# Performance work log

Hardware: AMD Instinct MI355X
Metric: run time of the kernel (lower is better)

## Reference

```python
import jax, jax.numpy as jnp
import numpy as np

B, T, C, H = 4, 2048, 1024, 16
D = C // H  # head_dim = 64

def setup_inputs() -> dict:
    key = jax.random.key(0)
    k1, k2, k3 = jax.random.split(key, 3)
    x = jax.random.normal(k1, (B, T, C), dtype=jnp.float32)
    Wqkv = jax.random.normal(k2, (C, 3 * C), dtype=jnp.float32) * (C ** -0.5)
    Wout = jax.random.normal(k3, (C, C), dtype=jnp.float32) * (C ** -0.5)
    return {"x": x, "Wqkv": Wqkv, "Wout": Wout}

def reference(x, Wqkv, Wout):
    b, t, c = x.shape
    scale = D ** -0.5
    qkv = x @ Wqkv  # [B,T,3C]
    q, k, v = jnp.split(qkv, 3, axis=-1)
    # [B,H,T,D]
    q = q.reshape(b, t, H, D).transpose(0, 2, 1, 3)
    k = k.reshape(b, t, H, D).transpose(0, 2, 1, 3)
    v = v.reshape(b, t, H, D).transpose(0, 2, 1, 3)
    scores = jnp.einsum('bhqd,bhkd->bhqk', q, k) * scale
    causal = jnp.tril(jnp.ones((t, t), dtype=bool))
    scores = jnp.where(causal, scores, -jnp.inf)
    attn = jax.nn.softmax(scores, axis=-1)
    out = jnp.einsum('bhqk,bhkd->bhqd', attn, v)
    out = out.transpose(0, 2, 1, 3).reshape(b, t, c)
    return out @ Wout
```

## Files before the change

kernel.cpp:

```cpp
#include <hip/hip_runtime.h>
#include <hip/hip_bf16.h>

#define DEV __device__ __forceinline__

typedef __attribute__((ext_vector_type(4))) float f32x4;
typedef __attribute__((ext_vector_type(8))) __bf16 bf16x8;
typedef __attribute__((ext_vector_type(8))) unsigned short u16x8;
typedef __attribute__((ext_vector_type(4))) unsigned short u16x4;

DEV unsigned short f2b(float x) {
  unsigned int u = __builtin_bit_cast(unsigned int, x);
  unsigned int r = (u + 0x7fffu + ((u >> 16) & 1u)) >> 16;
  return (unsigned short)r;
}

DEV unsigned int cvtpk(float a, float b) {
  unsigned int r;
  asm("v_cvt_pk_bf16_f32 %0, %1, %2" : "=v"(r) : "v"(a), "v"(b));
  return r;
}

DEV f32x4 mfma16(u16x8 a, u16x8 b, f32x4 c) {
  return __builtin_amdgcn_mfma_f32_16x16x32_bf16(
      __builtin_bit_cast(bf16x8, a), __builtin_bit_cast(bf16x8, b), c, 0, 0, 0);
}

DEV void async16(const unsigned short* g, unsigned short* l) {
  __builtin_amdgcn_global_load_lds(
      (const __attribute__((address_space(1))) void*)g,
      (__attribute__((address_space(3))) void*)l, 16, 0, 0);
}


__global__ void k_convert(const float* __restrict__ in, unsigned short* __restrict__ out, int n8) {
  int i = blockIdx.x * 256 + threadIdx.x;
  if (i >= n8) return;
  const float4* p = (const float4*)in + (size_t)i * 2;
  float4 a = p[0], b = p[1];
  u16x8 v;
  v[0] = f2b(a.x); v[1] = f2b(a.y); v[2] = f2b(a.z); v[3] = f2b(a.w);
  v[4] = f2b(b.x); v[5] = f2b(b.y); v[6] = f2b(b.z); v[7] = f2b(b.w);
  *((u16x8*)out + i) = v;
}

__global__ void k_transpose(const float* __restrict__ in, unsigned short* __restrict__ out,
                            int R, int Cc) {
  __shared__ float tile[32][33];
  int bx = blockIdx.x * 32, by = blockIdx.y * 32;
  int tx = threadIdx.x, ty = threadIdx.y;
#pragma unroll
  for (int i = 0; i < 32; i += 8)
    tile[ty + i][tx] = in[(size_t)(by + ty + i) * Cc + bx + tx];
  __syncthreads();
#pragma unroll
  for (int i = 0; i < 32; i += 8)
    out[(size_t)(bx + ty + i) * R + by + tx] = f2b(tile[tx][ty + i]);
}


template <typename OutT>
__global__ __launch_bounds__(256, 2)
void k_gemm_bt(const unsigned short* __restrict__ A, const unsigned short* __restrict__ Bt,
               OutT* __restrict__ C, int M, int N, int K, int ldc) {
  __shared__ __align__(16) unsigned short As[128 * 32];
  __shared__ __align__(16) unsigned short Bs[128 * 32];
  const int tid = threadIdx.x;
  const int w = tid >> 6, l = tid & 63;
  const int wr = w >> 1, wc = w & 1;
  const int lo = l & 15, hi = l >> 4;
  const int m0 = blockIdx.y * 128, n0 = blockIdx.x * 128;
  const int srow = l >> 2;
  const int scol = (l & 3) * 8;
  const size_t a_base = (size_t)(m0 + 2 * w * 16 + srow) * K + scol;
  const size_t b_base = (size_t)(n0 + 2 * w * 16 + srow) * K + scol;

  f32x4 acc[4][4] = {};

  for (int kt = 0; kt < K; kt += 32) {
    async16(A + a_base + kt, &As[(2 * w) * 512]);
    async16(A + a_base + kt + (size_t)16 * K, &As[(2 * w + 1) * 512]);
    async16(Bt + b_base + kt, &Bs[(2 * w) * 512]);
    async16(Bt + b_base + kt + (size_t)16 * K, &Bs[(2 * w + 1) * 512]);
    __syncthreads();
    u16x8 af[4], bfv[4];
#pragma unroll
    for (int mi = 0; mi < 4; ++mi)
      af[mi] = *(const u16x8*)&As[(wr * 64 + mi * 16 + lo) * 32 + hi * 8];
#pragma unroll
    for (int ni = 0; ni < 4; ++ni)
      bfv[ni] = *(const u16x8*)&Bs[(wc * 64 + ni * 16 + lo) * 32 + hi * 8];
#pragma unroll
    for (int mi = 0; mi < 4; ++mi)
#pragma unroll
      for (int ni = 0; ni < 4; ++ni)
        acc[mi][ni] = mfma16(af[mi], bfv[ni], acc[mi][ni]);
    __syncthreads();
  }
#pragma unroll
  for (int mi = 0; mi < 4; ++mi) {
#pragma unroll
    for (int ni = 0; ni < 4; ++ni) {
      int col = n0 + wc * 64 + ni * 16 + lo;
#pragma unroll
      for (int r = 0; r < 4; ++r) {
        int row = m0 + wr * 64 + mi * 16 + hi * 4 + r;
        float v = acc[mi][ni][r];
        if constexpr (sizeof(OutT) == 4)
          C[(size_t)row * ldc + col] = v;
        else
          C[(size_t)row * ldc + col] = f2b(v);
      }
    }
  }
}


__global__ void k_repack_qk(const unsigned short* __restrict__ qkv,
                            unsigned short* __restrict__ q, unsigned short* __restrict__ k) {
  int idx = blockIdx.x * 256 + threadIdx.x;
  int sel = idx >> 20;
  int rem = idx & ((1 << 20) - 1);
  int m = rem >> 7;
  int ch = rem & 127;
  int h = ch >> 3, d0 = (ch & 7) * 8;
  u16x8 v = *(const u16x8*)&qkv[(size_t)m * 3072 + sel * 1024 + h * 64 + d0];
  int b = m >> 11, t = m & 2047;
  unsigned short* dst = (sel == 0 ? q : k);
  *(u16x8*)&dst[(((size_t)(b * 16 + h)) * 2048 + t) * 64 + d0] = v;
}


__global__ void k_transpose_v(const unsigned short* __restrict__ qkv,
                              unsigned short* __restrict__ vt) {
  __shared__ __align__(16) unsigned short tile[64][68];
  int bh = blockIdx.x >> 5, tt = blockIdx.x & 31;
  int b = bh >> 4, h = bh & 15;
  int t0 = tt * 64;
  int tid = threadIdx.x;
  int rr = tid >> 4, cc = (tid & 15) * 4;
#pragma unroll
  for (int i = 0; i < 4; ++i) {
    int row = rr + i * 16;
    u16x4 v = *(const u16x4*)&qkv[(size_t)(b * 2048 + t0 + row) * 3072 + 2048 + h * 64 + cc];
    *(u16x4*)&tile[row][cc] = v;
  }
  __syncthreads();
  const int c32 = cc & 31;
  const int sbase = (c32 < 16) ? (2 * c32) : (2 * (c32 - 16) + 4);
  const int pos = t0 + (cc >> 5) * 32 + sbase;
#pragma unroll
  for (int i = 0; i < 4; ++i) {
    int d = rr + i * 16;
    u16x4 v;
#pragma unroll
    for (int j = 0; j < 4; ++j) v[j] = tile[cc + j][d];
    *(u16x4*)&vt[((size_t)bh * 64 + d) * 2048 + t0 + pos - t0] = v;
  }
}


DEV void attn_strip(const unsigned short* __restrict__ Q,
                    const unsigned short* __restrict__ Kp,
                    const unsigned short* __restrict__ Vp,
                    unsigned short* __restrict__ AO,
                    int bh, int q0, int lo, int g) {
  const size_t base = (size_t)bh * 2048 * 64;
  const unsigned short* Kb = Kp + base;
  const unsigned short* Vb = Vp + base;

  u16x8 qf[2][2];
#pragma unroll
  for (int qh = 0; qh < 2; ++qh)
#pragma unroll
    for (int dh = 0; dh < 2; ++dh)
      qf[qh][dh] = *(const u16x8*)&Q[base + (size_t)(q0 + qh * 16 + lo) * 64 + dh * 32 + g * 8];

  f32x4 o[2][4] = {};
  float m[2] = {-INFINITY, -INFINITY};
  float lsum[2] = {0.f, 0.f};

  const int nb = q0 / 32 + 1;
  u16x8 kA[2][2], kN[2][2];
#pragma unroll
  for (int kvh = 0; kvh < 2; ++kvh)
#pragma unroll
    for (int dh = 0; dh < 2; ++dh)
      kA[kvh][dh] = *(const u16x8*)&Kb[(size_t)(kvh * 16 + lo) * 64 + dh * 32 + g * 8];

  for (int blk = 0; blk < nb; ++blk) {
    const int kv0 = blk * 32;
    if (blk + 1 < nb) {
      const int kn = kv0 + 32;
#pragma unroll
      for (int kvh = 0; kvh < 2; ++kvh)
#pragma unroll
        for (int dh = 0; dh < 2; ++dh)
          kN[kvh][dh] = *(const u16x8*)&Kb[(size_t)(kn + kvh * 16 + lo) * 64 + dh * 32 + g * 8];
    }
    u16x8 vf[4];
#pragma unroll
    for (int n = 0; n < 4; ++n)
      vf[n] = *(const u16x8*)&Vb[(size_t)(n * 16 + lo) * 2048 + kv0 + g * 8];

    f32x4 sT[2][2];
#pragma unroll
    for (int qh = 0; qh < 2; ++qh)
#pragma unroll
      for (int kvh = 0; kvh < 2; ++kvh) {
        f32x4 z = {};
        z = mfma16(kA[kvh][0], qf[qh][0], z);
        z = mfma16(kA[kvh][1], qf[qh][1], z);
        sT[qh][kvh] = z;
      }

    const bool lastblk = (blk == nb - 1);
#pragma unroll
    for (int qh = 0; qh < 2; ++qh) {
      float s[8];
#pragma unroll
      for (int kvh = 0; kvh < 2; ++kvh)
#pragma unroll
        for (int r = 0; r < 4; ++r)
          s[kvh * 4 + r] = sT[qh][kvh][r] * 0.125f;
      if (lastblk) {
        const int qi = qh * 16 + lo;
#pragma unroll
        for (int kvh = 0; kvh < 2; ++kvh)
#pragma unroll
          for (int r = 0; r < 4; ++r)
            if (kvh * 16 + 4 * g + r > qi) s[kvh * 4 + r] = -INFINITY;
      }
      float mx = fmaxf(fmaxf(fmaxf(s[0], s[1]), fmaxf(s[2], s[3])),
                       fmaxf(fmaxf(s[4], s[5]), fmaxf(s[6], s[7])));
      mx = fmaxf(mx, __shfl_xor(mx, 16));
      mx = fmaxf(mx, __shfl_xor(mx, 32));
      float corr = 1.0f;
      if (!__all(mx <= m[qh] + 8.0f)) {
        float mn = fmaxf(m[qh], mx);
        corr = __expf(m[qh] - mn);
        m[qh] = mn;
#pragma unroll
        for (int n = 0; n < 4; ++n)
#pragma unroll
          for (int r = 0; r < 4; ++r) o[qh][n][r] *= corr;
      }
      float pe[8];
#pragma unroll
      for (int i = 0; i < 8; ++i) pe[i] = __expf(s[i] - m[qh]);
      float rs = ((pe[0] + pe[1]) + (pe[2] + pe[3])) + ((pe[4] + pe[5]) + (pe[6] + pe[7]));
      rs += __shfl_xor(rs, 16);
      rs += __shfl_xor(rs, 32);
      lsum[qh] = lsum[qh] * corr + rs;

      unsigned tw[4];
      tw[0] = cvtpk(pe[0], pe[1]);
      tw[1] = cvtpk(pe[2], pe[3]);
      tw[2] = cvtpk(pe[4], pe[5]);
      tw[3] = cvtpk(pe[6], pe[7]);
      u16x8 pB;
#pragma unroll
      for (int i = 0; i < 4; ++i) {
        pB[2 * i] = (unsigned short)(tw[i] & 0xffffu);
        pB[2 * i + 1] = (unsigned short)(tw[i] >> 16);
      }
#pragma unroll
      for (int n = 0; n < 4; ++n) o[qh][n] = mfma16(vf[n], pB, o[qh][n]);
    }

    if (blk + 1 < nb) {
#pragma unroll
      for (int kvh = 0; kvh < 2; ++kvh)
#pragma unroll
        for (int dh = 0; dh < 2; ++dh) kA[kvh][dh] = kN[kvh][dh];
    }
  }

  const int b = bh >> 4, h = bh & 15;
#pragma unroll
  for (int qh = 0; qh < 2; ++qh) {
    const float inv = 1.0f / lsum[qh];
    const int t = q0 + qh * 16 + lo;
    const size_t row = (size_t)(b * 2048 + t);
#pragma unroll
    for (int n = 0; n < 4; ++n) {
      u16x4 pk;
#pragma unroll
      for (int r = 0; r < 4; ++r) pk[r] = f2b(o[qh][n][r] * inv);
      *(u16x4*)&AO[row * 1024 + h * 64 + n * 16 + 4 * g] = pk;
    }
  }
}

__global__ __launch_bounds__(64)
void k_attn(const unsigned short* __restrict__ Q, const unsigned short* __restrict__ K,
            const unsigned short* __restrict__ V, unsigned short* __restrict__ AO) {
  const int l = threadIdx.x & 63;
  const int lo = l & 15, g = l >> 4;
  const int i = blockIdx.x;
  const int bh = (i & 7) * 8 + (i >> 8);
  const int p = (i >> 3) & 31;
  attn_strip(Q, K, V, AO, bh, p * 32, lo, g);
  attn_strip(Q, K, V, AO, bh, (63 - p) * 32, lo, g);
}


extern "C" void kernel_launch(void* const* d_in, const int* in_sizes, int n_in,
                              void* d_out, int out_size, void* d_ws, size_t ws_size,
                              hipStream_t stream) {
  (void)in_sizes; (void)n_in; (void)out_size;
  const float* x    = (const float*)d_in[0];
  const float* Wqkv = (const float*)d_in[1];
  const float* Wout = (const float*)d_in[2];
  float* out = (float*)d_out;

  const size_t OFF_XB  = 0;
  const size_t OFF_WQT = 16777216;
  const size_t OFF_WOT = 23068672;
  const size_t OFF_Q   = 25165824;
  const size_t OFF_K   = 41943040;
  const size_t OFF_VT  = 58720256;
  const size_t OFF_QKV = 75497472;
  const size_t NEED    = 125829120;
  if (ws_size < NEED) return;

  char* ws = (char*)d_ws;
  unsigned short* xb  = (unsigned short*)(ws + OFF_XB);
  unsigned short* wqT = (unsigned short*)(ws + OFF_WQT);
  unsigned short* woT = (unsigned short*)(ws + OFF_WOT);
  unsigned short* q   = (unsigned short*)(ws + OFF_Q);
  unsigned short* kk  = (unsigned short*)(ws + OFF_K);
  unsigned short* vt  = (unsigned short*)(ws + OFF_VT);
  unsigned short* qkv = (unsigned short*)(ws + OFF_QKV);
  unsigned short* ao  = qkv;

  k_convert<<<4096, 256, 0, stream>>>(x, xb, 1048576);
  dim3 tb(32, 8);
  k_transpose<<<dim3(96, 32), tb, 0, stream>>>(Wqkv, wqT, 1024, 3072);
  k_transpose<<<dim3(32, 32), tb, 0, stream>>>(Wout, woT, 1024, 1024);
  k_gemm_bt<unsigned short><<<dim3(24, 64), 256, 0, stream>>>(xb, wqT, qkv, 8192, 3072, 1024, 3072);
  k_repack_qk<<<8192, 256, 0, stream>>>(qkv, q, kk);
  k_transpose_v<<<2048, 256, 0, stream>>>(qkv, vt);
  k_attn<<<2048, 64, 0, stream>>>(q, kk, vt, ao);
  k_gemm_bt<float><<<dim3(8, 64), 256, 0, stream>>>(ao, woT, out, 8192, 1024, 1024, 1024);
}
```

Baseline: 245.7 us.

## Fuse QKV head repack and V transpose into GEMM epilogue; one strip per attention block

Adds a dedicated QKV GEMM whose epilogue writes Q and K directly in per-head layout and V in the transposed, permuted layout. This removes the separate repack and transpose kernels and the round trip through the intermediate qkv buffer. The attention launch now gives each block one causal strip, longest strips first, instead of a balanced pair, which doubles the block count. The epilogue writes for Q and K are scattered 2-byte stores that may coalesce poorly.

```diff
diff --git a/kernel.cpp b/kernel.cpp
--- a/kernel.cpp
+++ b/kernel.cpp
@@ -115,46 +115,70 @@
 }
 
 
-__global__ void k_repack_qk(const unsigned short* __restrict__ qkv,
-                            unsigned short* __restrict__ q, unsigned short* __restrict__ k) {
-  int idx = blockIdx.x * 256 + threadIdx.x;
-  int sel = idx >> 20;
-  int rem = idx & ((1 << 20) - 1);
-  int m = rem >> 7;
-  int ch = rem & 127;
-  int h = ch >> 3, d0 = (ch & 7) * 8;
-  u16x8 v = *(const u16x8*)&qkv[(size_t)m * 3072 + sel * 1024 + h * 64 + d0];
-  int b = m >> 11, t = m & 2047;
-  unsigned short* dst = (sel == 0 ? q : k);
-  *(u16x8*)&dst[(((size_t)(b * 16 + h)) * 2048 + t) * 64 + d0] = v;
-}
-
-
-__global__ void k_transpose_v(const unsigned short* __restrict__ qkv,
-                              unsigned short* __restrict__ vt) {
-  __shared__ __align__(16) unsigned short tile[64][68];
-  int bh = blockIdx.x >> 5, tt = blockIdx.x & 31;
-  int b = bh >> 4, h = bh & 15;
-  int t0 = tt * 64;
-  int tid = threadIdx.x;
-  int rr = tid >> 4, cc = (tid & 15) * 4;
-#pragma unroll
-  for (int i = 0; i < 4; ++i) {
-    int row = rr + i * 16;
-    u16x4 v = *(const u16x4*)&qkv[(size_t)(b * 2048 + t0 + row) * 3072 + 2048 + h * 64 + cc];
-    *(u16x4*)&tile[row][cc] = v;
-  }
-  __syncthreads();
-  const int c32 = cc & 31;
-  const int sbase = (c32 < 16) ? (2 * c32) : (2 * (c32 - 16) + 4);
-  const int pos = t0 + (cc >> 5) * 32 + sbase;
-#pragma unroll
-  for (int i = 0; i < 4; ++i) {
-    int d = rr + i * 16;
-    u16x4 v;
-#pragma unroll
-    for (int j = 0; j < 4; ++j) v[j] = tile[cc + j][d];
-    *(u16x4*)&vt[((size_t)bh * 64 + d) * 2048 + t0 + pos - t0] = v;
+__global__ __launch_bounds__(256, 2)
+void k_gemm_qkv(const unsigned short* __restrict__ A, const unsigned short* __restrict__ Bt,
+                unsigned short* __restrict__ q, unsigned short* __restrict__ kk,
+                unsigned short* __restrict__ vt) {
+  const int K = 1024;
+  __shared__ __align__(16) unsigned short As[128 * 32];
+  __shared__ __align__(16) unsigned short Bs[128 * 32];
+  const int tid = threadIdx.x;
+  const int w = tid >> 6, l = tid & 63;
+  const int wr = w >> 1, wc = w & 1;
+  const int lo = l & 15, hi = l >> 4;
+  const int m0 = blockIdx.y * 128, n0 = blockIdx.x * 128;
+  const int srow = l >> 2;
+  const int scol = (l & 3) * 8;
+  const size_t a_base = (size_t)(m0 + 2 * w * 16 + srow) * K + scol;
+  const size_t b_base = (size_t)(n0 + 2 * w * 16 + srow) * K + scol;
+
+  f32x4 acc[4][4] = {};
+
+  for (int kt = 0; kt < K; kt += 32) {
+    async16(A + a_base + kt, &As[(2 * w) * 512]);
+    async16(A + a_base + kt + (size_t)16 * K, &As[(2 * w + 1) * 512]);
+    async16(Bt + b_base + kt, &Bs[(2 * w) * 512]);
+    async16(Bt + b_base + kt + (size_t)16 * K, &Bs[(2 * w + 1) * 512]);
+    __syncthreads();
+    u16x8 af[4], bfv[4];
+#pragma unroll
+    for (int mi = 0; mi < 4; ++mi)
+      af[mi] = *(const u16x8*)&As[(wr * 64 + mi * 16 + lo) * 32 + hi * 8];
+#pragma unroll
+    for (int ni = 0; ni < 4; ++ni)
+      bfv[ni] = *(const u16x8*)&Bs[(wc * 64 + ni * 16 + lo) * 32 + hi * 8];
+#pragma unroll
+    for (int mi = 0; mi < 4; ++mi)
+#pragma unroll
+      for (int ni = 0; ni < 4; ++ni)
+        acc[mi][ni] = mfma16(af[mi], bfv[ni], acc[mi][ni]);
+    __syncthreads();
+  }
+#pragma unroll
+  for (int mi = 0; mi < 4; ++mi) {
+#pragma unroll
+    for (int ni = 0; ni < 4; ++ni) {
+      const int col = n0 + wc * 64 + ni * 16 + lo;
+      const int sel = col >> 10;
+      const int cc2 = col & 1023;
+      const int h = cc2 >> 6, d = cc2 & 63;
+      const int row0 = m0 + wr * 64 + mi * 16 + hi * 4;
+      const int b = row0 >> 11, t0q = row0 & 2047;
+      const int bh = b * 16 + h;
+      if (sel < 2) {
+        unsigned short* dst = (sel == 0) ? q : kk;
+#pragma unroll
+        for (int r = 0; r < 4; ++r)
+          dst[((size_t)bh * 2048 + t0q + r) * 64 + d] = f2b(acc[mi][ni][r]);
+      } else {
+        const int c32 = t0q & 31;
+        const int sbase = (c32 < 16) ? (2 * c32) : (2 * (c32 - 16) + 4);
+        u16x4 pk;
+#pragma unroll
+        for (int r = 0; r < 4; ++r) pk[r] = f2b(acc[mi][ni][r]);
+        *(u16x4*)&vt[((size_t)bh * 64 + d) * 2048 + (t0q & ~31) + sbase] = pk;
+      }
+    }
   }
 }
 
@@ -297,10 +321,10 @@
   const int l = threadIdx.x & 63;
   const int lo = l & 15, g = l >> 4;
   const int i = blockIdx.x;
-  const int bh = (i & 7) * 8 + (i >> 8);
-  const int p = (i >> 3) & 31;
-  attn_strip(Q, K, V, AO, bh, p * 32, lo, g);
-  attn_strip(Q, K, V, AO, bh, (63 - p) * 32, lo, g);
+  const int xcd = i & 7, j = i >> 3;
+  const int strip = 63 - (j & 63);
+  const int bh = xcd * 8 + (j >> 6);
+  attn_strip(Q, K, V, AO, bh, strip * 32, lo, g);
 }
 
 
@@ -319,7 +343,7 @@
   const size_t OFF_Q   = 25165824;
   const size_t OFF_K   = 41943040;
   const size_t OFF_VT  = 58720256;
-  const size_t OFF_QKV = 75497472;
+  const size_t OFF_AO  = 75497472;
   const size_t NEED    = 125829120;
   if (ws_size < NEED) return;
 
@@ -330,16 +354,13 @@
   unsigned short* q   = (unsigned short*)(ws + OFF_Q);
   unsigned short* kk  = (unsigned short*)(ws + OFF_K);
   unsigned short* vt  = (unsigned short*)(ws + OFF_VT);
-  unsigned short* qkv = (unsigned short*)(ws + OFF_QKV);
-  unsigned short* ao  = qkv;
+  unsigned short* ao  = (unsigned short*)(ws + OFF_AO);
 
   k_convert<<<4096, 256, 0, stream>>>(x, xb, 1048576);
   dim3 tb(32, 8);
   k_transpose<<<dim3(96, 32), tb, 0, stream>>>(Wqkv, wqT, 1024, 3072);
   k_transpose<<<dim3(32, 32), tb, 0, stream>>>(Wout, woT, 1024, 1024);
-  k_gemm_bt<unsigned short><<<dim3(24, 64), 256, 0, stream>>>(xb, wqT, qkv, 8192, 3072, 1024, 3072);
-  k_repack_qk<<<8192, 256, 0, stream>>>(qkv, q, kk);
-  k_transpose_v<<<2048, 256, 0, stream>>>(qkv, vt);
-  k_attn<<<2048, 64, 0, stream>>>(q, kk, vt, ao);
+  k_gemm_qkv<<<dim3(24, 64), 256, 0, stream>>>(xb, wqT, q, kk, vt);
+  k_attn<<<4096, 64, 0, stream>>>(q, kk, vt, ao);
   k_gemm_bt<float><<<dim3(8, 64), 256, 0, stream>>>(ao, woT, out, 8192, 1024, 1024, 1024);
 }
```

New measurement: 262.7 us. 6.9% more time.
